# Kernel optimization log

Hardware: AMD Instinct MI355X
Metric: run time of the kernel (lower is better)

Reference implementation:

```python
import jax, jax.numpy as jnp
import numpy as np

DEPTH = 3
B, D, O = 8192, 1024, 1024
HR = 32            # router hidden
HE = 2 * D         # expert hidden
N_NODES = 2 ** DEPTH - 1
N_LEAVES = 2 ** DEPTH


def setup_inputs() -> dict:
    key = jax.random.key(0)
    ks = jax.random.split(key, 9)
    x = jax.random.normal(ks[0], (B, D), dtype=jnp.float32)
    # decision-node router params (stacked over nodes)
    rW1 = jax.random.normal(ks[1], (N_NODES, D, HR), dtype=jnp.float32) * 0.05
    rb1 = jnp.zeros((N_NODES, HR), dtype=jnp.float32)
    rW2 = jax.random.normal(ks[2], (N_NODES, HR, 2), dtype=jnp.float32) * 0.05
    rb2 = jnp.zeros((N_NODES, 2), dtype=jnp.float32)
    # leaf-expert params (stacked over experts)
    eW1 = jax.random.normal(ks[3], (N_LEAVES, D, HE), dtype=jnp.float32) * 0.02
    eb1 = jnp.zeros((N_LEAVES, HE), dtype=jnp.float32)
    eW2 = jax.random.normal(ks[4], (N_LEAVES, HE, O), dtype=jnp.float32) * 0.02
    eb2 = jnp.zeros((N_LEAVES, O), dtype=jnp.float32)
    return {"x": x, "rW1": rW1, "rb1": rb1, "rW2": rW2, "rb2": rb2,
            "eW1": eW1, "eb1": eb1, "eW2": eW2, "eb2": eb2, "top_k": 4}


def _gelu(v):
    return jax.nn.gelu(v, approximate=False)  # torch nn.GELU default = exact erf


def _leaf_probs(x, rW1, rb1, rW2, rb2):
    # all decision nodes batched: [N, B, 2]
    h = _gelu(jnp.einsum('bd,ndh->nbh', x, rW1) + rb1[:, None, :])
    logits = jnp.einsum('nbh,nhc->nbc', h, rW2) + rb2[:, None, :]
    dec = jax.nn.softmax(logits, axis=-1)
    # BFS product of path probabilities, level by level (fixed small loop)
    probs = jnp.ones((x.shape[0], 1), dtype=x.dtype)
    start = 0
    for level in range(DEPTH):
        w = 2 ** level
        dl = dec[start:start + w].transpose(1, 0, 2)       # [B, w, 2]
        probs = (probs[:, :, None] * dl).reshape(x.shape[0], 2 * w)
        start += w
    return probs  # [B, N_LEAVES]


def reference(x, rW1, rb1, rW2, rb2, eW1, eb1, eW2, eb2, top_k):
    leaf_probs = _leaf_probs(x, rW1, rb1, rW2, rb2)
    if top_k is not None and top_k < N_LEAVES:
        vals, idx = jax.lax.top_k(leaf_probs, top_k)       # [B, k]
        sparse = jnp.zeros_like(leaf_probs)
        sparse = sparse.at[jnp.arange(leaf_probs.shape[0])[:, None], idx].set(vals)
        leaf_probs = sparse / (sparse.sum(axis=1, keepdims=True) + 1e-8)
    # all leaf experts, batched (dense weighted sum; skip heuristic is an approximation)
    h = _gelu(jnp.einsum('bd,edh->ebh', x, eW1) + eb1[:, None, :])   # [E, B, HE]
    out = jnp.einsum('ebh,eho->ebo', h, eW2) + eb2[:, None, :]        # [E, B, O]
    y = jnp.einsum('ebo,be->bo', out, leaf_probs)
    return (y, leaf_probs)
```

## Files before the change

kernel.cpp:

```cpp
#include <hip/hip_runtime.h>
#include <hip/hip_bf16.h>
#include <cstdint>

#define B_   8192
#define D_   1024
#define O_   1024
#define HE_  2048
#define NN_  7
#define NL_  8
#define HR_  32
#define RC_  224
#define K3_  3072
#define MTMAX_ 264

typedef __attribute__((ext_vector_type(2))) float f32x2;
typedef __attribute__((ext_vector_type(4))) float f32x4;
typedef __attribute__((ext_vector_type(8))) short bf16x8;
typedef __attribute__((ext_vector_type(4))) unsigned short u16x4;
typedef unsigned short u16;
typedef unsigned int u32;

__device__ __forceinline__ u16 f2bf(float f) {
  __hip_bfloat16 h = __float2bfloat16(f);
  return *reinterpret_cast<u16*>(&h);
}
__device__ __forceinline__ float bf2f(u16 u) {
  u32 v = ((u32)u) << 16;
  return *reinterpret_cast<float*>(&v);
}
__device__ __forceinline__ float gelu_exact(float v) {
  return 0.5f * v * (1.0f + erff(v * 0.7071067811865475f));
}
__device__ __forceinline__ void gload16(const void* g, void* l) {
  __builtin_amdgcn_global_load_lds(
      (const __attribute__((address_space(1))) void*)(uintptr_t)g,
      (__attribute__((address_space(3))) void*)(uintptr_t)l,
      16, 0, 0);
}
#define WAITVM0   asm volatile("s_waitcnt vmcnt(0)" ::: "memory")
#define WAITLGKM0 do { \
  asm volatile("s_waitcnt lgkmcnt(0)" ::: "memory"); \
  __builtin_amdgcn_sched_barrier(0); } while (0)

__global__ __launch_bounds__(256) void build_xbs_kernel(
    const float* __restrict__ in, u16* __restrict__ out) {
  size_t i = ((size_t)blockIdx.x * 256 + threadIdx.x) * 4;
  size_t row = i >> 10;
  int col = (int)(i & 1023);
  f32x4 f = *reinterpret_cast<const f32x4*>(in + i);
  u16x4 hi, lo;
#pragma unroll
  for (int j = 0; j < 4; j++) {
    hi[j] = f2bf(f[j]);
    lo[j] = f2bf(f[j] - bf2f(hi[j]));
  }
  u16* base = out + row * 2048 + col;
  *reinterpret_cast<u16x4*>(base)        = hi;
  *reinterpret_cast<u16x4*>(base + 1024) = lo;
}

__global__ __launch_bounds__(256) void build_wr3_kernel(
    const float* __restrict__ rW1, u16* __restrict__ Wr3) {
  size_t i = ((size_t)blockIdx.x * 256 + threadIdx.x) * 4;
  int c = (int)(i / K3_), k = (int)(i % K3_);
  int j = k >> 10, kk = k & 1023;
  u16x4 o;
  if (c < RC_) {
    int node = c >> 5, h = c & 31;
    const float* src = rW1 + ((size_t)node * 1024 + kk) * HR_ + h;
#pragma unroll
    for (int t = 0; t < 4; t++) {
      float f = src[t * HR_];
      u16 hi = f2bf(f);
      o[t] = (j == 1) ? f2bf(f - bf2f(hi)) : hi;
    }
  } else {
    o[0] = 0; o[1] = 0; o[2] = 0; o[3] = 0;
  }
  *reinterpret_cast<u16x4*>(Wr3 + i) = o;
}

__global__ __launch_bounds__(256) void transpose_cvt_kernel(
    const float* __restrict__ in, u16* __restrict__ out,
    int R, int C, int ldo, long in_estride, long out_estride) {
  __shared__ __attribute__((aligned(16))) float tile[64][65];
  const float* in_e = in + (long)blockIdx.z * in_estride;
  u16* out_e = out + (long)blockIdx.z * out_estride;
  int t = threadIdx.x;
  int r0 = blockIdx.y * 64, c0 = blockIdx.x * 64;
  int cc = t & 63, rbase = t >> 6;
#pragma unroll
  for (int i = 0; i < 16; i++) {
    int rr = rbase + i * 4;
    tile[rr][cc] = in_e[(long)(r0 + rr) * C + c0 + cc];
  }
  __syncthreads();
  int r2 = (t & 31) * 2, cj = t >> 5;
#pragma unroll
  for (int i = 0; i < 8; i++) {
    int c = cj * 8 + i;
    u32 u = (u32)f2bf(tile[r2][c]) | ((u32)f2bf(tile[r2 + 1][c]) << 16);
    *reinterpret_cast<u32*>(out_e + (long)(c0 + c) * ldo + r0 + r2) = u;
  }
}

__global__ __launch_bounds__(256, 2) void router_gemm_kernel(
    const u16* __restrict__ Xbs, const u16* __restrict__ Bm,
    float* __restrict__ H1p) {
  __shared__ __attribute__((aligned(16))) u16 lA[128 * 32];
  __shared__ __attribute__((aligned(16))) u16 lB[128 * 32];
  int tid = threadIdx.x;
  int gid = blockIdx.x;
  int cpx = gridDim.x >> 3;
  gid = (gid & 7) * cpx + (gid >> 3);
  int s = gid >> 7;
  int rem = gid & 127;
  int band = rem >> 4, inb = rem & 15;
  long m0 = (long)(band * 8 + (inb & 7)) * 128;
  long n0 = (long)(inb >> 3) * 128;
  int wid = tid >> 6, lane = tid & 63;
  int wm = wid >> 1, wn = wid & 1;
  f32x4 acc[4][4];
#pragma unroll
  for (int m = 0; m < 4; m++)
#pragma unroll
    for (int n = 0; n < 4; n++) acc[m][n] = (f32x4){0.f, 0.f, 0.f, 0.f};
  int lr = lane & 15, lk = (lane >> 4) * 8;
  int srow = tid >> 2, soff = (tid & 3) * 8;
  const u16* Bb = Bm + n0 * K3_;
  int kbeg = s * 768, kend = kbeg + 768;
  for (int k0 = kbeg; k0 < kend; k0 += 32) {
    int ca = (k0 < 1024) ? k0 : k0 - 1024;
    gload16(Xbs + (m0 + srow) * 2048 + ca + soff, &lA[tid * 8]);
    gload16(Xbs + (m0 + 64 + srow) * 2048 + ca + soff, &lA[(256 + tid) * 8]);
    gload16(Bb + (long)srow * K3_ + k0 + soff, &lB[tid * 8]);
    gload16(Bb + (long)(64 + srow) * K3_ + k0 + soff, &lB[(256 + tid) * 8]);
    __syncthreads();
    bf16x8 af[4], bfr[4];
#pragma unroll
    for (int m = 0; m < 4; m++)
      af[m] = *reinterpret_cast<const bf16x8*>(&lA[(wm * 64 + m * 16 + lr) * 32 + lk]);
#pragma unroll
    for (int n = 0; n < 4; n++)
      bfr[n] = *reinterpret_cast<const bf16x8*>(&lB[(wn * 64 + n * 16 + lr) * 32 + lk]);
#pragma unroll
    for (int m = 0; m < 4; m++)
#pragma unroll
      for (int n = 0; n < 4; n++)
        acc[m][n] = __builtin_amdgcn_mfma_f32_16x16x32_bf16(af[m], bfr[n], acc[m][n], 0, 0, 0);
    __syncthreads();
  }
  int lq = lane >> 4;
#pragma unroll
  for (int m = 0; m < 4; m++)
#pragma unroll
    for (int n = 0; n < 4; n++)
#pragma unroll
      for (int j = 0; j < 4; j++) {
        long row = m0 + wm * 64 + m * 16 + lq * 4 + j;
        long col = n0 + wn * 64 + n * 16 + lr;
        if (col < RC_)
          H1p[((long)s * B_ + row) * RC_ + col] = acc[m][n][j];
      }
}

__global__ __launch_bounds__(256) void router_logits_kernel(
    const float* __restrict__ H1p, const float* __restrict__ rb1,
    const float* __restrict__ rW2, const float* __restrict__ rb2,
    const int* __restrict__ topk_ptr, float* __restrict__ P) {
  int b = blockIdx.x * 256 + threadIdx.x;
  float dec[NN_][2];
#pragma unroll
  for (int n = 0; n < NN_; n++) {
    float l0 = rb2[n * 2], l1 = rb2[n * 2 + 1];
#pragma unroll
    for (int r4 = 0; r4 < HR_; r4 += 4) {
      int c = n * HR_ + r4;
      f32x4 hs = *reinterpret_cast<const f32x4*>(&H1p[((long)0 * B_ + b) * RC_ + c]);
#pragma unroll
      for (int s = 1; s < 4; s++)
        hs += *reinterpret_cast<const f32x4*>(&H1p[((long)s * B_ + b) * RC_ + c]);
      f32x4 bv = *reinterpret_cast<const f32x4*>(rb1 + c);
#pragma unroll
      for (int j = 0; j < 4; j++) {
        float hv = gelu_exact(hs[j] + bv[j]);
        l0 += hv * rW2[(c + j) * 2];
        l1 += hv * rW2[(c + j) * 2 + 1];
      }
    }
    float mx = fmaxf(l0, l1);
    float e0 = expf(l0 - mx), e1 = expf(l1 - mx);
    float sm = e0 + e1;
    dec[n][0] = e0 / sm; dec[n][1] = e1 / sm;
  }
  float v[NL_];
#pragma unroll
  for (int L = 0; L < NL_; L++)
    v[L] = dec[0][L >> 2] * dec[1 + (L >> 2)][(L >> 1) & 1] * dec[3 + (L >> 1)][L & 1];
  int tk = *topk_ptr;
  float p[NL_];
  if (tk < NL_) {
    float s = 0.f;
    bool keep[NL_];
#pragma unroll
    for (int e = 0; e < NL_; e++) {
      int rank = 0;
#pragma unroll
      for (int j = 0; j < NL_; j++)
        rank += ((v[j] > v[e]) || (v[j] == v[e] && j < e)) ? 1 : 0;
      keep[e] = rank < tk;
      if (keep[e]) s += v[e];
    }
    float inv = 1.f / (s + 1e-8f);
#pragma unroll
    for (int e = 0; e < NL_; e++) p[e] = keep[e] ? v[e] * inv : 0.f;
  } else {
#pragma unroll
    for (int e = 0; e < NL_; e++) p[e] = v[e];
  }
#pragma unroll
  for (int e = 0; e < NL_; e++) P[(long)b * NL_ + e] = p[e];
}

__global__ __launch_bounds__(256) void yinit_kernel(
    const float* __restrict__ P, const float* __restrict__ eb2,
    float* __restrict__ y) {
  size_t i = ((size_t)blockIdx.x * 256 + threadIdx.x) * 4;
  size_t row = i >> 10;
  int col = (int)(i & 1023);
  f32x4 s = (f32x4){0.f, 0.f, 0.f, 0.f};
#pragma unroll
  for (int e = 0; e < NL_; e++) {
    float pe = P[row * NL_ + e];
    f32x4 w = *reinterpret_cast<const f32x4*>(eb2 + (size_t)e * O_ + col);
    s += w * pe;
  }
  *reinterpret_cast<f32x4*>(y + i) = s;
}

__global__ __launch_bounds__(256) void compact_kernel(
    const float* __restrict__ P, int* __restrict__ idx,
    int* __restrict__ counts) {
  int e = blockIdx.x, t = threadIdx.x;
  __shared__ int sc[256];
  __shared__ int sbase;
  if (t == 0) sbase = 0;
  __syncthreads();
  for (int c0 = 0; c0 < B_; c0 += 256) {
    int r = c0 + t;
    int f = (P[(long)r * NL_ + e] > 0.f) ? 1 : 0;
    sc[t] = f;
    __syncthreads();
#pragma unroll
    for (int d = 1; d < 256; d <<= 1) {
      int v = (t >= d) ? sc[t - d] : 0;
      __syncthreads();
      sc[t] += v;
      __syncthreads();
    }
    int pos = sbase + sc[t] - 1;
    int tot = sc[255];
    if (f) idx[(long)e * B_ + pos] = r;
    __syncthreads();
    if (t == 0) sbase += tot;
    __syncthreads();
  }
  if (t == 0) counts[e] = sbase;
}

__global__ void tiles_kernel(const int* __restrict__ counts,
                             int* __restrict__ toff) {
  int s = 0;
#pragma unroll
  for (int e = 0; e < NL_; e++) { toff[e] = s; s += (counts[e] + 127) >> 7; }
  toff[NL_] = s;
}

__global__ __launch_bounds__(256, 2) void gemme1_kernel(
    const u16* __restrict__ Xbs, const u16* __restrict__ W1t,
    const float* __restrict__ eb1, const float* __restrict__ P,
    u16* __restrict__ Hall, const int* __restrict__ idx,
    const int* __restrict__ counts, const int* __restrict__ toff) {
  __shared__ __attribute__((aligned(16))) u16 lA[2][128 * 64];
  __shared__ __attribute__((aligned(16))) u16 lB[2][128 * 64];
  int tid = threadIdx.x;
  int gid = blockIdx.x;
  int cpx = gridDim.x >> 3;
  gid = (gid & 7) * cpx + (gid >> 3);
  int mt = gid >> 4, nt = gid & 15;
  if (mt >= toff[NL_]) return;
  int e = 0;
#pragma unroll
  for (int f = 1; f < NL_; f++) e += (mt >= toff[f]) ? 1 : 0;
  int cnt = counts[e];
  long m0 = (long)(mt - toff[e]) * 128;
  long n0 = (long)nt * 128;
  const int* idxe = idx + (long)e * B_;
  int wid = tid >> 6, lane = tid & 63;
  int wm = wid >> 1, wn = wid & 1;
  f32x4 acc[4][4];
#pragma unroll
  for (int m = 0; m < 4; m++)
#pragma unroll
    for (int n = 0; n < 4; n++) acc[m][n] = (f32x4){0.f, 0.f, 0.f, 0.f};
  int lr = lane & 15, lkg = lane >> 4;
  const u16* gA[4]; const u16* gB[4]; int lds_o[4];
  const u16* Bb = W1t + ((size_t)e * HE_ + n0) * D_;
#pragma unroll
  for (int i = 0; i < 4; i++) {
    int sidx = tid + i * 256;
    int r = sidx >> 3, j = sidx & 7;
    int so = ((j ^ (r & 7)) << 3);
    int gi = (m0 + r < cnt) ? idxe[m0 + r] : 0;
    gA[i] = Xbs + (long)gi * 2048 + so;
    gB[i] = Bb + (long)r * D_ + so;
    lds_o[i] = sidx * 8;
  }
  int foA[4][2], foB[4][2];
#pragma unroll
  for (int m = 0; m < 4; m++) {
    int r = wm * 64 + m * 16 + lr;
#pragma unroll
    for (int kk = 0; kk < 2; kk++)
      foA[m][kk] = r * 128 + ((((kk * 4 + lkg) ^ (r & 7))) << 4);
  }
#pragma unroll
  for (int n = 0; n < 4; n++) {
    int r = wn * 64 + n * 16 + lr;
#pragma unroll
    for (int kk = 0; kk < 2; kk++)
      foB[n][kk] = r * 128 + ((((kk * 4 + lkg) ^ (r & 7))) << 4);
  }
#define STAGE1(buf, k0) do { _Pragma("unroll") \
  for (int i_ = 0; i_ < 4; i_++) gload16(gA[i_] + (k0), &lA[buf][lds_o[i_]]); \
  _Pragma("unroll") \
  for (int i_ = 0; i_ < 4; i_++) gload16(gB[i_] + (k0), &lB[buf][lds_o[i_]]); \
  } while (0)
  STAGE1(0, 0);
  WAITVM0;
  __builtin_amdgcn_s_barrier();
  int cur = 0;
  constexpr int NT = D_ / 64;
  for (int t = 0; t < NT; ++t) {
    if (t + 1 < NT) STAGE1(cur ^ 1, (t + 1) * 64);
    const char* pa = (const char*)lA[cur];
    const char* pb = (const char*)lB[cur];
    bf16x8 af[4][2], bfr[4][2];
#pragma unroll
    for (int m = 0; m < 4; m++) {
      af[m][0] = *reinterpret_cast<const bf16x8*>(pa + foA[m][0]);
      af[m][1] = *reinterpret_cast<const bf16x8*>(pa + foA[m][1]);
    }
#pragma unroll
    for (int n = 0; n < 4; n++) {
      bfr[n][0] = *reinterpret_cast<const bf16x8*>(pb + foB[n][0]);
      bfr[n][1] = *reinterpret_cast<const bf16x8*>(pb + foB[n][1]);
    }
    WAITLGKM0;
    __builtin_amdgcn_s_setprio(1);
#pragma unroll
    for (int m = 0; m < 4; m++)
#pragma unroll
      for (int n = 0; n < 4; n++) {
        acc[m][n] = __builtin_amdgcn_mfma_f32_16x16x32_bf16(af[m][0], bfr[n][0], acc[m][n], 0, 0, 0);
        acc[m][n] = __builtin_amdgcn_mfma_f32_16x16x32_bf16(af[m][1], bfr[n][1], acc[m][n], 0, 0, 0);
      }
    __builtin_amdgcn_s_setprio(0);
    WAITVM0;
    __builtin_amdgcn_s_barrier();
    cur ^= 1;
  }
#undef STAGE1
  int lq = lane >> 4;
  long hbase = (long)toff[e] * 128;
#pragma unroll
  for (int m = 0; m < 4; m++) {
#pragma unroll
    for (int j = 0; j < 4; j++) {
      long lrow = m0 + wm * 64 + m * 16 + lq * 4 + j;
      if (lrow >= cnt) continue;
      int orow = idxe[lrow];
      float pw = P[(long)orow * NL_ + e];
#pragma unroll
      for (int n = 0; n < 4; n++) {
        long col = n0 + wn * 64 + n * 16 + lr;
        float g = gelu_exact(acc[m][n][j] + eb1[(size_t)e * HE_ + col]);
        Hall[(hbase + lrow) * HE_ + col] = f2bf(g * pw);
      }
    }
  }
}

__global__ __launch_bounds__(256, 2) void gemme2_kernel(
    const u16* __restrict__ Hall, const u16* __restrict__ W2t,
    float* __restrict__ y, const int* __restrict__ idx,
    const int* __restrict__ counts, const int* __restrict__ toff) {
  __shared__ __attribute__((aligned(16))) u16 lA[2][128 * 64];
  __shared__ __attribute__((aligned(16))) u16 lB[2][128 * 64];
  int tid = threadIdx.x;
  int gid = blockIdx.x;
  int cpx = gridDim.x >> 3;
  gid = (gid & 7) * cpx + (gid >> 3);
  int mt = gid >> 3, nt = gid & 7;
  if (mt >= toff[NL_]) return;
  int e = 0;
#pragma unroll
  for (int f = 1; f < NL_; f++) e += (mt >= toff[f]) ? 1 : 0;
  int cnt = counts[e];
  long m0 = (long)(mt - toff[e]) * 128;
  long n0 = (long)nt * 128;
  const int* idxe = idx + (long)e * B_;
  int wid = tid >> 6, lane = tid & 63;
  int wm = wid >> 1, wn = wid & 1;
  f32x4 acc[4][4];
#pragma unroll
  for (int m = 0; m < 4; m++)
#pragma unroll
    for (int n = 0; n < 4; n++) acc[m][n] = (f32x4){0.f, 0.f, 0.f, 0.f};
  int lr = lane & 15, lkg = lane >> 4;
  const u16* Ab = Hall + ((long)toff[e] * 128 + m0) * HE_;
  const u16* Bb = W2t + ((size_t)e * O_ + n0) * HE_;
  const u16* gA[4]; const u16* gB[4]; int lds_o[4];
#pragma unroll
  for (int i = 0; i < 4; i++) {
    int sidx = tid + i * 256;
    int r = sidx >> 3, j = sidx & 7;
    int so = ((j ^ (r & 7)) << 3);
    gA[i] = Ab + (long)r * HE_ + so;
    gB[i] = Bb + (long)r * HE_ + so;
    lds_o[i] = sidx * 8;
  }
  int foA[4][2], foB[4][2];
#pragma unroll
  for (int m = 0; m < 4; m++) {
    int r = wm * 64 + m * 16 + lr;
#pragma unroll
    for (int kk = 0; kk < 2; kk++)
      foA[m][kk] = r * 128 + ((((kk * 4 + lkg) ^ (r & 7))) << 4);
  }
#pragma unroll
  for (int n = 0; n < 4; n++) {
    int r = wn * 64 + n * 16 + lr;
#pragma unroll
    for (int kk = 0; kk < 2; kk++)
      foB[n][kk] = r * 128 + ((((kk * 4 + lkg) ^ (r & 7))) << 4);
  }
#define STAGE2(buf, k0) do { _Pragma("unroll") \
  for (int i_ = 0; i_ < 4; i_++) gload16(gA[i_] + (k0), &lA[buf][lds_o[i_]]); \
  _Pragma("unroll") \
  for (int i_ = 0; i_ < 4; i_++) gload16(gB[i_] + (k0), &lB[buf][lds_o[i_]]); \
  } while (0)
  STAGE2(0, 0);
  WAITVM0;
  __builtin_amdgcn_s_barrier();
  int cur = 0;
  constexpr int NT = HE_ / 64;
  for (int t = 0; t < NT; ++t) {
    if (t + 1 < NT) STAGE2(cur ^ 1, (t + 1) * 64);
    const char* pa = (const char*)lA[cur];
    const char* pb = (const char*)lB[cur];
    bf16x8 af[4][2], bfr[4][2];
#pragma unroll
    for (int m = 0; m < 4; m++) {
      af[m][0] = *reinterpret_cast<const bf16x8*>(pa + foA[m][0]);
      af[m][1] = *reinterpret_cast<const bf16x8*>(pa + foA[m][1]);
    }
#pragma unroll
    for (int n = 0; n < 4; n++) {
      bfr[n][0] = *reinterpret_cast<const bf16x8*>(pb + foB[n][0]);
      bfr[n][1] = *reinterpret_cast<const bf16x8*>(pb + foB[n][1]);
    }
    WAITLGKM0;
    __builtin_amdgcn_s_setprio(1);
#pragma unroll
    for (int m = 0; m < 4; m++)
#pragma unroll
      for (int n = 0; n < 4; n++) {
        acc[m][n] = __builtin_amdgcn_mfma_f32_16x16x32_bf16(af[m][0], bfr[n][0], acc[m][n], 0, 0, 0);
        acc[m][n] = __builtin_amdgcn_mfma_f32_16x16x32_bf16(af[m][1], bfr[n][1], acc[m][n], 0, 0, 0);
      }
    __builtin_amdgcn_s_setprio(0);
    WAITVM0;
    __builtin_amdgcn_s_barrier();
    cur ^= 1;
  }
#undef STAGE2
  int lq = lane >> 4;
#pragma unroll
  for (int m = 0; m < 4; m++) {
#pragma unroll
    for (int j = 0; j < 4; j++) {
      long lrow = m0 + wm * 64 + m * 16 + lq * 4 + j;
      if (lrow >= cnt) continue;
      long orow = idxe[lrow];
#pragma unroll
      for (int n = 0; n < 4; n++) {
        long col = n0 + wn * 64 + n * 16 + lr;
        unsafeAtomicAdd(&y[orow * O_ + col], acc[m][n][j]);
      }
    }
  }
}

extern "C" void kernel_launch(void* const* d_in, const int* in_sizes, int n_in,
                              void* d_out, int out_size, void* d_ws, size_t ws_size,
                              hipStream_t stream) {
  (void)in_sizes; (void)n_in; (void)out_size; (void)ws_size;
  const float* x   = (const float*)d_in[0];
  const float* rW1 = (const float*)d_in[1];
  const float* rb1 = (const float*)d_in[2];
  const float* rW2 = (const float*)d_in[3];
  const float* rb2 = (const float*)d_in[4];
  const float* eW1 = (const float*)d_in[5];
  const float* eb1 = (const float*)d_in[6];
  const float* eW2 = (const float*)d_in[7];
  const float* eb2 = (const float*)d_in[8];
  const int*  topk = (const int*)d_in[9];
  float* y = (float*)d_out;
  float* P = y + (size_t)B_ * O_;

  char* ws = (char*)d_ws;
  u16*  Xbs = (u16*)ws;
  u16*  W1t = (u16*)(ws + 33554432);
  u16*  W2t = (u16*)(ws + 67108864);
  int*  idx    = (int*)(ws + 100663296);
  int*  counts = (int*)(ws + 100925440);
  int*  toff   = (int*)(ws + 100925504);
  char* hreg   = ws + 100925952;
  u16*  Hall = (u16*)hreg;
  u16*  Wr3  = (u16*)hreg;
  float* H1p = (float*)(hreg + 2097152);

  build_xbs_kernel<<<(B_ * D_) / 1024, 256, 0, stream>>>(x, Xbs);
  build_wr3_kernel<<<(256 * K3_) / 1024, 256, 0, stream>>>(rW1, Wr3);
  transpose_cvt_kernel<<<dim3(HE_ / 64, D_ / 64, NL_), 256, 0, stream>>>(
      eW1, W1t, D_, HE_, D_, (long)D_ * HE_, (long)HE_ * D_);
  transpose_cvt_kernel<<<dim3(O_ / 64, HE_ / 64, NL_), 256, 0, stream>>>(
      eW2, W2t, HE_, O_, HE_, (long)HE_ * O_, (long)O_ * HE_);
  router_gemm_kernel<<<512, 256, 0, stream>>>(Xbs, Wr3, H1p);
  router_logits_kernel<<<B_ / 256, 256, 0, stream>>>(H1p, rb1, rW2, rb2, topk, P);
  yinit_kernel<<<(B_ * O_) / 1024, 256, 0, stream>>>(P, eb2, y);
  compact_kernel<<<NL_, 256, 0, stream>>>(P, idx, counts);
  tiles_kernel<<<1, 1, 0, stream>>>(counts, toff);

  gemme1_kernel<<<MTMAX_ * 16, 256, 0, stream>>>(
      Xbs, W1t, eb1, P, Hall, idx, counts, toff);
  gemme2_kernel<<<MTMAX_ * 8, 256, 0, stream>>>(
      Hall, W2t, y, idx, counts, toff);
}
```

Before: 720.5 us.

## Use ballot-based compaction, drop tiles kernel, rework GEMM pipelining in expert kernels

Replaces the LDS Hillis-Steele scan in compaction with wave ballot and popcount prefix sums, cutting many barriers. Removes the separate tiles kernel by computing tile offsets from counts inside each GEMM block. Switches gemme1 to a single-buffered loop with __syncthreads, and changes gemme2 to wait with vmcnt(8) so the next stage's loads stay in flight during compute. The single-buffered gemme1 loses load/compute overlap but uses less LDS, which may allow higher occupancy.

```diff
diff --git a/kernel.cpp b/kernel.cpp
--- a/kernel.cpp
+++ b/kernel.cpp
@@ -37,10 +37,28 @@
       (__attribute__((address_space(3))) void*)(uintptr_t)l,
       16, 0, 0);
 }
-#define WAITVM0   asm volatile("s_waitcnt vmcnt(0)" ::: "memory")
+#define WAITVM(n) asm volatile("s_waitcnt vmcnt(" #n ")" ::: "memory")
 #define WAITLGKM0 do { \
   asm volatile("s_waitcnt lgkmcnt(0)" ::: "memory"); \
   __builtin_amdgcn_sched_barrier(0); } while (0)
+
+__device__ __forceinline__ bool expert_of_tile(
+    const int* __restrict__ counts, int mt,
+    int& e, int& cnt, long& m0, long& hbase) {
+  int tot = 0; e = -1; cnt = 0; int tofe = 0;
+#pragma unroll
+  for (int f = 0; f < NL_; f++) {
+    int c = counts[f];
+    int tl = (c + 127) >> 7;
+    bool in = (e < 0) && (mt < tot + tl);
+    if (in) { e = f; tofe = tot; cnt = c; }
+    tot += tl;
+  }
+  if (e < 0) return false;
+  m0 = (long)(mt - tofe) * 128;
+  hbase = (long)tofe * 128;
+  return true;
+}
 
 __global__ __launch_bounds__(256) void build_xbs_kernel(
     const float* __restrict__ in, u16* __restrict__ out) {
@@ -242,58 +260,44 @@
     const float* __restrict__ P, int* __restrict__ idx,
     int* __restrict__ counts) {
   int e = blockIdx.x, t = threadIdx.x;
-  __shared__ int sc[256];
+  int wave = t >> 6, lane = t & 63;
+  __shared__ int wsum[4];
   __shared__ int sbase;
   if (t == 0) sbase = 0;
   __syncthreads();
   for (int c0 = 0; c0 < B_; c0 += 256) {
     int r = c0 + t;
-    int f = (P[(long)r * NL_ + e] > 0.f) ? 1 : 0;
-    sc[t] = f;
-    __syncthreads();
-#pragma unroll
-    for (int d = 1; d < 256; d <<= 1) {
-      int v = (t >= d) ? sc[t - d] : 0;
-      __syncthreads();
-      sc[t] += v;
-      __syncthreads();
-    }
-    int pos = sbase + sc[t] - 1;
-    int tot = sc[255];
-    if (f) idx[(long)e * B_ + pos] = r;
+    bool f = P[(long)r * NL_ + e] > 0.f;
+    unsigned long long mask = __ballot(f);
+    int intra = __popcll(mask & ((1ULL << lane) - 1ULL));
+    if (lane == 0) wsum[wave] = __popcll(mask);
+    __syncthreads();
+    int wpre = 0;
+#pragma unroll
+    for (int w = 0; w < 4; w++) wpre += (w < wave) ? wsum[w] : 0;
+    int tot = wsum[0] + wsum[1] + wsum[2] + wsum[3];
+    if (f) idx[(long)e * B_ + sbase + wpre + intra] = r;
     __syncthreads();
     if (t == 0) sbase += tot;
     __syncthreads();
   }
   if (t == 0) counts[e] = sbase;
-}
-
-__global__ void tiles_kernel(const int* __restrict__ counts,
-                             int* __restrict__ toff) {
-  int s = 0;
-#pragma unroll
-  for (int e = 0; e < NL_; e++) { toff[e] = s; s += (counts[e] + 127) >> 7; }
-  toff[NL_] = s;
 }
 
 __global__ __launch_bounds__(256, 2) void gemme1_kernel(
     const u16* __restrict__ Xbs, const u16* __restrict__ W1t,
     const float* __restrict__ eb1, const float* __restrict__ P,
     u16* __restrict__ Hall, const int* __restrict__ idx,
-    const int* __restrict__ counts, const int* __restrict__ toff) {
-  __shared__ __attribute__((aligned(16))) u16 lA[2][128 * 64];
-  __shared__ __attribute__((aligned(16))) u16 lB[2][128 * 64];
+    const int* __restrict__ counts) {
+  __shared__ __attribute__((aligned(16))) u16 lA[128 * 64];
+  __shared__ __attribute__((aligned(16))) u16 lB[128 * 64];
   int tid = threadIdx.x;
   int gid = blockIdx.x;
   int cpx = gridDim.x >> 3;
   gid = (gid & 7) * cpx + (gid >> 3);
   int mt = gid >> 4, nt = gid & 15;
-  if (mt >= toff[NL_]) return;
-  int e = 0;
-#pragma unroll
-  for (int f = 1; f < NL_; f++) e += (mt >= toff[f]) ? 1 : 0;
-  int cnt = counts[e];
-  long m0 = (long)(mt - toff[e]) * 128;
+  int e, cnt; long m0, hbase;
+  if (!expert_of_tile(counts, mt, e, cnt, m0, hbase)) return;
   long n0 = (long)nt * 128;
   const int* idxe = idx + (long)e * B_;
   int wid = tid >> 6, lane = tid & 63;
@@ -331,20 +335,14 @@
     for (int kk = 0; kk < 2; kk++)
       foB[n][kk] = r * 128 + ((((kk * 4 + lkg) ^ (r & 7))) << 4);
   }
-#define STAGE1(buf, k0) do { _Pragma("unroll") \
-  for (int i_ = 0; i_ < 4; i_++) gload16(gA[i_] + (k0), &lA[buf][lds_o[i_]]); \
-  _Pragma("unroll") \
-  for (int i_ = 0; i_ < 4; i_++) gload16(gB[i_] + (k0), &lB[buf][lds_o[i_]]); \
-  } while (0)
-  STAGE1(0, 0);
-  WAITVM0;
-  __builtin_amdgcn_s_barrier();
-  int cur = 0;
-  constexpr int NT = D_ / 64;
-  for (int t = 0; t < NT; ++t) {
-    if (t + 1 < NT) STAGE1(cur ^ 1, (t + 1) * 64);
-    const char* pa = (const char*)lA[cur];
-    const char* pb = (const char*)lB[cur];
+  const char* pa = (const char*)lA;
+  const char* pb = (const char*)lB;
+  for (int k0 = 0; k0 < D_; k0 += 64) {
+#pragma unroll
+    for (int i = 0; i < 4; i++) gload16(gA[i] + k0, &lA[lds_o[i]]);
+#pragma unroll
+    for (int i = 0; i < 4; i++) gload16(gB[i] + k0, &lB[lds_o[i]]);
+    __syncthreads();
     bf16x8 af[4][2], bfr[4][2];
 #pragma unroll
     for (int m = 0; m < 4; m++) {
@@ -356,8 +354,6 @@
       bfr[n][0] = *reinterpret_cast<const bf16x8*>(pb + foB[n][0]);
       bfr[n][1] = *reinterpret_cast<const bf16x8*>(pb + foB[n][1]);
     }
-    WAITLGKM0;
-    __builtin_amdgcn_s_setprio(1);
 #pragma unroll
     for (int m = 0; m < 4; m++)
 #pragma unroll
@@ -365,14 +361,9 @@
         acc[m][n] = __builtin_amdgcn_mfma_f32_16x16x32_bf16(af[m][0], bfr[n][0], acc[m][n], 0, 0, 0);
         acc[m][n] = __builtin_amdgcn_mfma_f32_16x16x32_bf16(af[m][1], bfr[n][1], acc[m][n], 0, 0, 0);
       }
-    __builtin_amdgcn_s_setprio(0);
-    WAITVM0;
-    __builtin_amdgcn_s_barrier();
-    cur ^= 1;
-  }
-#undef STAGE1
+    __syncthreads();
+  }
   int lq = lane >> 4;
-  long hbase = (long)toff[e] * 128;
 #pragma unroll
   for (int m = 0; m < 4; m++) {
 #pragma unroll
@@ -394,7 +385,7 @@
 __global__ __launch_bounds__(256, 2) void gemme2_kernel(
     const u16* __restrict__ Hall, const u16* __restrict__ W2t,
     float* __restrict__ y, const int* __restrict__ idx,
-    const int* __restrict__ counts, const int* __restrict__ toff) {
+    const int* __restrict__ counts) {
   __shared__ __attribute__((aligned(16))) u16 lA[2][128 * 64];
   __shared__ __attribute__((aligned(16))) u16 lB[2][128 * 64];
   int tid = threadIdx.x;
@@ -402,12 +393,8 @@
   int cpx = gridDim.x >> 3;
   gid = (gid & 7) * cpx + (gid >> 3);
   int mt = gid >> 3, nt = gid & 7;
-  if (mt >= toff[NL_]) return;
-  int e = 0;
-#pragma unroll
-  for (int f = 1; f < NL_; f++) e += (mt >= toff[f]) ? 1 : 0;
-  int cnt = counts[e];
-  long m0 = (long)(mt - toff[e]) * 128;
+  int e, cnt; long m0, hbase;
+  if (!expert_of_tile(counts, mt, e, cnt, m0, hbase)) return;
   long n0 = (long)nt * 128;
   const int* idxe = idx + (long)e * B_;
   int wid = tid >> 6, lane = tid & 63;
@@ -418,7 +405,7 @@
 #pragma unroll
     for (int n = 0; n < 4; n++) acc[m][n] = (f32x4){0.f, 0.f, 0.f, 0.f};
   int lr = lane & 15, lkg = lane >> 4;
-  const u16* Ab = Hall + ((long)toff[e] * 128 + m0) * HE_;
+  const u16* Ab = Hall + (hbase + m0) * HE_;
   const u16* Bb = W2t + ((size_t)e * O_ + n0) * HE_;
   const u16* gA[4]; const u16* gB[4]; int lds_o[4];
 #pragma unroll
@@ -451,12 +438,17 @@
   for (int i_ = 0; i_ < 4; i_++) gload16(gB[i_] + (k0), &lB[buf][lds_o[i_]]); \
   } while (0)
   STAGE2(0, 0);
-  WAITVM0;
-  __builtin_amdgcn_s_barrier();
   int cur = 0;
   constexpr int NT = HE_ / 64;
   for (int t = 0; t < NT; ++t) {
-    if (t + 1 < NT) STAGE2(cur ^ 1, (t + 1) * 64);
+    if (t + 1 < NT) {
+      STAGE2(cur ^ 1, (t + 1) * 64);
+      WAITVM(8);
+    } else {
+      WAITVM(0);
+    }
+    __builtin_amdgcn_s_barrier();
+    __builtin_amdgcn_sched_barrier(0);
     const char* pa = (const char*)lA[cur];
     const char* pb = (const char*)lB[cur];
     bf16x8 af[4][2], bfr[4][2];
@@ -480,8 +472,8 @@
         acc[m][n] = __builtin_amdgcn_mfma_f32_16x16x32_bf16(af[m][1], bfr[n][1], acc[m][n], 0, 0, 0);
       }
     __builtin_amdgcn_s_setprio(0);
-    WAITVM0;
     __builtin_amdgcn_s_barrier();
+    __builtin_amdgcn_sched_barrier(0);
     cur ^= 1;
   }
 #undef STAGE2
@@ -525,7 +517,6 @@
   u16*  W2t = (u16*)(ws + 67108864);
   int*  idx    = (int*)(ws + 100663296);
   int*  counts = (int*)(ws + 100925440);
-  int*  toff   = (int*)(ws + 100925504);
   char* hreg   = ws + 100925952;
   u16*  Hall = (u16*)hreg;
   u16*  Wr3  = (u16*)hreg;
@@ -541,10 +532,9 @@
   router_logits_kernel<<<B_ / 256, 256, 0, stream>>>(H1p, rb1, rW2, rb2, topk, P);
   yinit_kernel<<<(B_ * O_) / 1024, 256, 0, stream>>>(P, eb2, y);
   compact_kernel<<<NL_, 256, 0, stream>>>(P, idx, counts);
-  tiles_kernel<<<1, 1, 0, stream>>>(counts, toff);
 
   gemme1_kernel<<<MTMAX_ * 16, 256, 0, stream>>>(
-      Xbs, W1t, eb1, P, Hall, idx, counts, toff);
+      Xbs, W1t, eb1, P, Hall, idx, counts);
   gemme2_kernel<<<MTMAX_ * 8, 256, 0, stream>>>(
-      Hall, W2t, y, idx, counts, toff);
-}
+      Hall, W2t, y, idx, counts);
+}
```

Result: faster. 638.2 us (-11.4%).
